# Performance work log

Hardware: AMD Instinct MI355X
Metric: run time of the kernel (lower is better)

Reference implementation:

```python
import jax, jax.numpy as jnp
import numpy as np


def setup_inputs() -> dict:
    key = jax.random.key(0)
    ks = jax.random.split(key, 5)
    N, D, H, E = 8192, 1024, 4096, 8
    s = 0.02
    return {
        "x": jax.random.normal(ks[0], (N, D), jnp.float32),
        "Wr": jax.random.normal(ks[1], (D, E), jnp.float32) * s,
        "br": jnp.zeros((E,), jnp.float32),
        "W1": jax.random.normal(ks[2], (E, D, H), jnp.float32) * s,
        "b1": jnp.zeros((E, H), jnp.float32),
        "W2": jax.random.normal(ks[3], (E, H, D), jnp.float32) * s,
        "b2": jnp.zeros((E, D), jnp.float32),
        "k": 2,
    }


def reference(x, Wr, br, W1, b1, W2, b2, k):
    # Router (eval mode: no gate noise)
    logits = x @ Wr + br                      # [N, E]
    scores = jax.nn.softmax(logits, axis=-1)  # [N, E]
    topk_vals, topk_inds = jax.lax.top_k(scores, k)  # [N, k]
    N, E = scores.shape
    # dispatch_mask: zeros scattered with top-k probabilities
    dispatch_mask = jnp.zeros_like(scores).at[
        jnp.arange(N)[:, None], topk_inds
    ].set(topk_vals)                          # [N, E]
    # Dense all-expert FFN compute (faithful to the original wasteful pattern)
    h = jax.nn.relu(jnp.einsum('nd,edh->neh', x, W1) + b1)   # [N, E, H]
    expert_outputs = jnp.einsum('neh,ehd->ned', h, W2) + b2  # [N, E, D]
    output = jnp.einsum('ned,ne->nd', expert_outputs, dispatch_mask)  # [N, D]
    # Load-balancing aux loss (torch.var is unbiased, ddof=1)
    importance = dispatch_mask.sum(axis=0)    # [E]
    imp_mean = jnp.mean(importance)
    imp_var = jnp.var(importance, ddof=1)
    aux_loss = imp_var / (imp_mean ** 2 + 1e-9)
    return output, aux_loss
```

## Files before the change

kernel.cpp:

```cpp
#include <hip/hip_runtime.h>
#include <hip/hip_bf16.h>


#define NTOK 8192
#define DDIM 1024
#define HDIM 4096
#define NEXP 8
#define NASSIGN (NTOK * 2)
#define MAX_MT 72
#define GRID1 (16 * MAX_MT)
#define GRID2A (4 * 2 * MAX_MT)
#define GRID2B (4 * MAX_MT)

typedef __bf16 bf16_t;
typedef __bf16 bf16x2 __attribute__((ext_vector_type(2)));
typedef __bf16 bf16x4 __attribute__((ext_vector_type(4)));
typedef __bf16 bf16x8 __attribute__((ext_vector_type(8)));
typedef float f32x4 __attribute__((ext_vector_type(4)));

#define GLOAD16(gptr, lptr)                                                    \
  __builtin_amdgcn_global_load_lds(                                            \
      (const __attribute__((address_space(1))) void*)(gptr),                   \
      (__attribute__((address_space(3))) void*)(lptr), 16, 0, 0)

#define VMCNT0 asm volatile("s_waitcnt vmcnt(0)" ::: "memory")

#define MFMA16(a, b, c) __builtin_amdgcn_mfma_f32_16x16x32_bf16(a, b, c, 0, 0, 0)

__device__ __forceinline__ int xcd_swz(int orig, int nwg) {
  const int cpx = nwg >> 3;
  return (orig & 7) * cpx + (orig >> 3);
}

__global__ void __launch_bounds__(256) transpose_cvt_kernel(
    const float* __restrict__ in, bf16_t* __restrict__ out, int R, int C) {
  __shared__ float tile[64][33];
  const size_t mat = (size_t)R * C;
  const float* ip = in + (size_t)blockIdx.z * mat;
  bf16_t* op = out + (size_t)blockIdx.z * mat;
  const int c0 = blockIdx.x * 32, r0 = blockIdx.y * 64;
  const int tx = threadIdx.x, ty = threadIdx.y;
#pragma unroll
  for (int i = 0; i < 8; ++i) {
    const int r = ty + 8 * i;
    tile[r][tx] = ip[(size_t)(r0 + r) * C + (c0 + tx)];
  }
  __syncthreads();
#pragma unroll
  for (int j = 0; j < 4; ++j) {
    const int c = ty + 8 * j;
    bf16x2 v;
    v[0] = (bf16_t)tile[2 * tx][c];
    v[1] = (bf16_t)tile[2 * tx + 1][c];
    *(bf16x2*)(op + (size_t)(c0 + c) * R + r0 + 2 * tx) = v;
  }
}

__global__ void __launch_bounds__(256) router_kernel(
    const float* __restrict__ x, const float* __restrict__ Wr,
    const float* __restrict__ br, int2* __restrict__ ids,
    float2* __restrict__ prs, int* __restrict__ counts,
    bf16_t* __restrict__ xb) {
  const int n = blockIdx.x;
  const int t = threadIdx.x;
  const int wave = t >> 6, lane = t & 63;
  const float4 xv = ((const float4*)(x + (size_t)n * DDIM))[t];
  bf16x4 o;
  o[0] = (bf16_t)xv.x; o[1] = (bf16_t)xv.y;
  o[2] = (bf16_t)xv.z; o[3] = (bf16_t)xv.w;
  ((bf16x4*)(xb + (size_t)n * DDIM))[t] = o;

  float acc[NEXP];
#pragma unroll
  for (int e = 0; e < NEXP; ++e) acc[e] = 0.f;
  const float xq[4] = {xv.x, xv.y, xv.z, xv.w};
#pragma unroll
  for (int q = 0; q < 4; ++q) {
    const float* w = Wr + (size_t)(4 * t + q) * NEXP;
#pragma unroll
    for (int e = 0; e < NEXP; ++e) acc[e] += xq[q] * w[e];
  }
#pragma unroll
  for (int off = 32; off >= 1; off >>= 1)
#pragma unroll
    for (int e = 0; e < NEXP; ++e) acc[e] += __shfl_down(acc[e], off);
  __shared__ float red[4][NEXP];
  if (lane == 0)
#pragma unroll
    for (int e = 0; e < NEXP; ++e) red[wave][e] = acc[e];
  __syncthreads();
  if (t == 0) {
    float l[NEXP];
#pragma unroll
    for (int e = 0; e < NEXP; ++e)
      l[e] = ((red[0][e] + red[1][e]) + (red[2][e] + red[3][e])) + br[e];
    int i1 = 0; float v1 = l[0];
    for (int e = 1; e < NEXP; ++e)
      if (l[e] > v1) { v1 = l[e]; i1 = e; }
    int i2 = (i1 == 0) ? 1 : 0; float v2 = l[i2];
    for (int e = 0; e < NEXP; ++e)
      if (e != i1 && l[e] > v2) { v2 = l[e]; i2 = e; }
    float denom = 0.f;
    for (int e = 0; e < NEXP; ++e) denom += expf(l[e] - v1);
    ids[n] = make_int2(i1, i2);
    prs[n] = make_float2(1.f / denom, expf(v2 - v1) / denom);
    atomicAdd(&counts[i1], 1);
    atomicAdd(&counts[i2], 1);
  }
}

__global__ void __launch_bounds__(256) scan_aux_kernel(
    const int* __restrict__ counts, int* __restrict__ offsets,
    int* __restrict__ tmap, const int2* __restrict__ ids,
    const float2* __restrict__ prs, float* __restrict__ aux_out) {
  const int t = threadIdx.x;
  if (t == 0) {
    int off = 0, nt = 0;
    for (int e = 0; e < NEXP; ++e) {
      offsets[e] = off;
      const int c = counts[e];
      for (int m0 = 0; m0 < c; m0 += 256) {
        tmap[nt] = e;
        tmap[MAX_MT + nt] = m0;
        ++nt;
      }
      off += c;
    }
    offsets[NEXP] = off;
    tmap[2 * MAX_MT] = nt;
  }
  float imp[NEXP];
#pragma unroll
  for (int e = 0; e < NEXP; ++e) imp[e] = 0.f;
  for (int n = t; n < NTOK; n += 256) {
    const int2 id = ids[n];
    const float2 pr = prs[n];
#pragma unroll
    for (int e = 0; e < NEXP; ++e)
      imp[e] += (id.x == e ? pr.x : 0.f) + (id.y == e ? pr.y : 0.f);
  }
  __shared__ float red[256][NEXP];
#pragma unroll
  for (int e = 0; e < NEXP; ++e) red[t][e] = imp[e];
  __syncthreads();
  for (int s = 128; s >= 1; s >>= 1) {
    if (t < s) {
#pragma unroll
      for (int e = 0; e < NEXP; ++e) red[t][e] += red[t + s][e];
    }
    __syncthreads();
  }
  if (t == 0) {
    float m = 0.f;
    for (int e = 0; e < NEXP; ++e) m += red[0][e];
    m *= (1.f / NEXP);
    float v = 0.f;
    for (int e = 0; e < NEXP; ++e) {
      const float d = red[0][e] - m;
      v += d * d;
    }
    v *= (1.f / (NEXP - 1));
    aux_out[0] = v / (m * m + 1e-9f);
  }
}

__global__ void __launch_bounds__(256) scatter_kernel(
    const int2* __restrict__ ids, const float2* __restrict__ prs,
    const int* __restrict__ offsets, int* __restrict__ cursor,
    int* __restrict__ btok, float* __restrict__ bprob,
    int2* __restrict__ amap) {
  const int n = blockIdx.x * 256 + threadIdx.x;
  if (n >= NTOK) return;
  const int2 id = ids[n];
  const float2 pr = prs[n];
  int p = atomicAdd(&cursor[id.x], 1);
  const int a1 = offsets[id.x] + p;
  btok[a1] = n;
  bprob[a1] = pr.x;
  p = atomicAdd(&cursor[id.y], 1);
  const int a2 = offsets[id.y] + p;
  btok[a2] = n;
  bprob[a2] = pr.y;
  amap[n] = make_int2(a1, a2);
}

__global__ void __launch_bounds__(256) combine_kernel(
    const float* __restrict__ o0, const float* __restrict__ o1,
    const int2* __restrict__ amap, const float* __restrict__ bprob,
    float* __restrict__ out) {
  const int n = blockIdx.x;
  const int d = threadIdx.x * 4;
  const int2 a = amap[n];
  const float p1 = bprob[a.x], p2 = bprob[a.y];
  const float4 u0 = *(const float4*)(o0 + (size_t)a.x * DDIM + d);
  const float4 u1 = *(const float4*)(o1 + (size_t)a.x * DDIM + d);
  const float4 v0 = *(const float4*)(o0 + (size_t)a.y * DDIM + d);
  const float4 v1 = *(const float4*)(o1 + (size_t)a.y * DDIM + d);
  float4 r;
  r.x = p1 * (u0.x + u1.x) + p2 * (v0.x + v1.x);
  r.y = p1 * (u0.y + u1.y) + p2 * (v0.y + v1.y);
  r.z = p1 * (u0.z + u1.z) + p2 * (v0.z + v1.z);
  r.w = p1 * (u0.w + u1.w) + p2 * (v0.w + v1.w);
  *(float4*)(out + (size_t)n * DDIM + d) = r;
}


#define STAGE_A(BUF, KO)                                                       \
  GLOAD16(asrc0 + (KO), (char*)Al + (BUF)*32768 + 0*8192 + wave*1024);         \
  GLOAD16(asrc1 + (KO), (char*)Al + (BUF)*32768 + 1*8192 + wave*1024);         \
  GLOAD16(asrc2 + (KO), (char*)Al + (BUF)*32768 + 2*8192 + wave*1024);         \
  GLOAD16(asrc3 + (KO), (char*)Al + (BUF)*32768 + 3*8192 + wave*1024);

#define STAGE_B(BUF, KO)                                                       \
  GLOAD16(bsrc0 + (KO), (char*)Bl + (BUF)*32768 + 0*8192 + wave*1024);         \
  GLOAD16(bsrc1 + (KO), (char*)Bl + (BUF)*32768 + 1*8192 + wave*1024);         \
  GLOAD16(bsrc2 + (KO), (char*)Bl + (BUF)*32768 + 2*8192 + wave*1024);         \
  GLOAD16(bsrc3 + (KO), (char*)Bl + (BUF)*32768 + 3*8192 + wave*1024);

#define LOAD_AF(O0, O1, O2, O3, KX)                                            \
  af0 = *(const bf16x8*)(Ac + ((O0) ^ (KX)));                                  \
  af1 = *(const bf16x8*)(Ac + ((O1) ^ (KX)));                                  \
  af2 = *(const bf16x8*)(Ac + ((O2) ^ (KX)));                                  \
  af3 = *(const bf16x8*)(Ac + ((O3) ^ (KX)));

#define LOAD_BF(KX)                                                            \
  bf0 = *(const bf16x8*)(Bc + (boffb0 ^ (KX)));                                \
  bf1 = *(const bf16x8*)(Bc + (boffb1 ^ (KX)));                                \
  bf2 = *(const bf16x8*)(Bc + (boffb2 ^ (KX)));                                \
  bf3 = *(const bf16x8*)(Bc + (boffb3 ^ (KX)));

#define MROW(M, A)                                                             \
  acc[M][0] = MFMA16(A, bf0, acc[M][0]);                                       \
  acc[M][1] = MFMA16(A, bf1, acc[M][1]);                                       \
  acc[M][2] = MFMA16(A, bf2, acc[M][2]);                                       \
  acc[M][3] = MFMA16(A, bf3, acc[M][3]);

#define PH_MFMA(MB)                                                            \
  __builtin_amdgcn_s_setprio(1);                                               \
  MROW(MB + 0, af0) MROW(MB + 1, af1) MROW(MB + 2, af2) MROW(MB + 3, af3)      \
  __builtin_amdgcn_s_setprio(0);

#define PH_ENTER                                                               \
  __builtin_amdgcn_sched_barrier(0x1);                                         \
  __builtin_amdgcn_s_barrier();

#define PH_EXIT __builtin_amdgcn_s_barrier();

#define KLOOP(NT)                                                              \
  STAGE_A(0, 0)                                                                \
  STAGE_B(0, 0)                                                                \
  VMCNT0;                                                                      \
  __builtin_amdgcn_s_barrier();                                                \
  __builtin_amdgcn_sched_barrier(0);                                           \
  _Pragma("unroll 2") for (int t = 0; t < (NT); ++t) {                         \
    const int cb = t & 1, nc = cb ^ 1;                                         \
    const int ko = (t + 1) * 64;                                               \
    const char* Ac = (const char*)Al + cb * 32768;                             \
    const char* Bc = (const char*)Bl + cb * 32768;                             \
    const bool pf = (t + 1 < (NT));                                            \
    bf16x8 af0, af1, af2, af3, bf0, bf1, bf2, bf3;                             \
                               \
    LOAD_AF(aoffb0, aoffb1, aoffb2, aoffb3, 0)                                 \
    LOAD_BF(0)                                                                 \
    if (pf) { STAGE_A(nc, ko) }                                                \
    PH_ENTER                                                                   \
    PH_MFMA(0)                                                                 \
    PH_EXIT                                                                    \
                                        \
    LOAD_AF(aoffb4, aoffb5, aoffb6, aoffb7, 0)                                 \
    if (pf) { STAGE_B(nc, ko) }                                                \
    PH_ENTER                                                                   \
    PH_MFMA(4)                                                                 \
    PH_EXIT                                                                    \
                                             \
    LOAD_AF(aoffb0, aoffb1, aoffb2, aoffb3, 64)                                \
    LOAD_BF(64)                                                                \
    PH_ENTER                                                                   \
    PH_MFMA(0)                                                                 \
    PH_EXIT                                                                    \
                                 \
    LOAD_AF(aoffb4, aoffb5, aoffb6, aoffb7, 64)                                \
    PH_ENTER                                                                   \
    PH_MFMA(4)                                                                 \
    VMCNT0;                                                                    \
    __builtin_amdgcn_s_barrier();                                              \
    __builtin_amdgcn_sched_barrier(0);                                         \
  }

#define GEOM_SETUP                                                             \
  const int tid = threadIdx.x;                                                 \
  const int wave = tid >> 6;                                                   \
  const int lane = tid & 63;                                                   \
  const int wr = (wave >> 2) * 128;                                            \
  const int wc = (wave & 3) * 64;                                              \
  const int lrow = lane & 15;                                                  \
  const int lslot = lane >> 4;                                                 \
  const int sxor = ((lslot ^ (lrow & 7)) << 4);                                \
  const int aoffb0 = (wr + 0 * 16 + lrow) * 128 + sxor;                        \
  const int aoffb1 = (wr + 1 * 16 + lrow) * 128 + sxor;                        \
  const int aoffb2 = (wr + 2 * 16 + lrow) * 128 + sxor;                        \
  const int aoffb3 = (wr + 3 * 16 + lrow) * 128 + sxor;                        \
  const int aoffb4 = (wr + 4 * 16 + lrow) * 128 + sxor;                        \
  const int aoffb5 = (wr + 5 * 16 + lrow) * 128 + sxor;                        \
  const int aoffb6 = (wr + 6 * 16 + lrow) * 128 + sxor;                        \
  const int aoffb7 = (wr + 7 * 16 + lrow) * 128 + sxor;                        \
  const int boffb0 = (wc + 0 * 16 + lrow) * 128 + sxor;                        \
  const int boffb1 = (wc + 1 * 16 + lrow) * 128 + sxor;                        \
  const int boffb2 = (wc + 2 * 16 + lrow) * 128 + sxor;                        \
  const int boffb3 = (wc + 3 * 16 + lrow) * 128 + sxor;

#define SRC_ROW(S) ((S)*64 + (tid >> 3))
#define SRC_SLOT ((tid & 7))

__global__ void __launch_bounds__(512, 2) gemm1_kernel(
    const bf16_t* __restrict__ xb, const bf16_t* __restrict__ W1t,
    const float* __restrict__ b1, const int* __restrict__ btok,
    const int* __restrict__ offsets, const int* __restrict__ counts,
    const int* __restrict__ tmap, bf16_t* __restrict__ h) {
  const int job = xcd_swz((int)blockIdx.x, GRID1);
  const int tidx = job >> 4;
  const int nblk = job & 15;
  if (tidx >= tmap[2 * MAX_MT]) return;
  const int e = tmap[tidx];
  const int m0 = tmap[MAX_MT + tidx];
  const int cnt = counts[e];
  const int aoff = offsets[e];
  const int n0 = nblk * 256;

  __shared__ __align__(16) bf16_t Al[2][256 * 64];
  __shared__ __align__(16) bf16_t Bl[2][256 * 64];

  GEOM_SETUP

  const bf16_t *asrc0, *asrc1, *asrc2, *asrc3;
  const bf16_t *bsrc0, *bsrc1, *bsrc2, *bsrc3;
  {
    const int p = SRC_SLOT;
#pragma unroll
    for (int s = 0; s < 4; ++s) {
      const int row = SRC_ROW(s);
      const int l = p ^ (row & 7);
      int arow = m0 + row;
      if (arow > cnt - 1) arow = cnt - 1;
      const bf16_t* ap = xb + (size_t)btok[aoff + arow] * DDIM + l * 8;
      const bf16_t* bp = W1t + ((size_t)e * HDIM + n0 + row) * DDIM + l * 8;
      if (s == 0) { asrc0 = ap; bsrc0 = bp; }
      else if (s == 1) { asrc1 = ap; bsrc1 = bp; }
      else if (s == 2) { asrc2 = ap; bsrc2 = bp; }
      else { asrc3 = ap; bsrc3 = bp; }
    }
  }

  f32x4 acc[8][4];
#pragma unroll
  for (int mf = 0; mf < 8; ++mf)
#pragma unroll
    for (int nf = 0; nf < 4; ++nf) acc[mf][nf] = (f32x4){0.f, 0.f, 0.f, 0.f};

  KLOOP(16)

  const int rbase = (lane >> 4) * 4;
  const float* b1e = b1 + (size_t)e * HDIM + n0;
#pragma unroll
  for (int nf = 0; nf < 4; ++nf) {
    const int cl = wc + nf * 16 + lrow;
    const float bb = b1e[cl];
#pragma unroll
    for (int mf = 0; mf < 8; ++mf) {
#pragma unroll
      for (int r = 0; r < 4; ++r) {
        const int grow = wr + mf * 16 + rbase + r;
        if (m0 + grow < cnt)
          h[(size_t)(aoff + m0 + grow) * HDIM + (n0 + cl)] =
              (bf16_t)fmaxf(acc[mf][nf][r] + bb, 0.f);
      }
    }
  }
}

template <int NT, int KSP, bool ATOMIC>
__global__ void __launch_bounds__(512, 2) gemm2_kernel(
    const bf16_t* __restrict__ h, const bf16_t* __restrict__ W2t,
    const float* __restrict__ b2, const int* __restrict__ btok,
    const float* __restrict__ bprob, const int* __restrict__ offsets,
    const int* __restrict__ counts, const int* __restrict__ tmap,
    float* __restrict__ o0, float* __restrict__ o1,
    float* __restrict__ out) {
  const int nwg = 4 * KSP * MAX_MT;
  const int job = xcd_swz((int)blockIdx.x, nwg);
  const int tidx = job / (4 * KSP);
  const int rem = job % (4 * KSP);
  const int nblk = rem & 3;
  const int kch = rem >> 2;
  if (tidx >= tmap[2 * MAX_MT]) return;
  const int e = tmap[tidx];
  const int m0 = tmap[MAX_MT + tidx];
  const int cnt = counts[e];
  const int aoff = offsets[e];
  const int n0 = nblk * 256;
  const int kbase = kch * (HDIM / KSP);

  __shared__ __align__(16) bf16_t Al[2][256 * 64];
  __shared__ __align__(16) bf16_t Bl[2][256 * 64];

  GEOM_SETUP

  const bf16_t *asrc0, *asrc1, *asrc2, *asrc3;
  const bf16_t *bsrc0, *bsrc1, *bsrc2, *bsrc3;
  {
    const int p = SRC_SLOT;
#pragma unroll
    for (int s = 0; s < 4; ++s) {
      const int row = SRC_ROW(s);
      const int l = p ^ (row & 7);
      int arow = m0 + row;
      if (arow > cnt - 1) arow = cnt - 1;
      const bf16_t* ap = h + (size_t)(aoff + arow) * HDIM + kbase + l * 8;
      const bf16_t* bp =
          W2t + ((size_t)e * DDIM + n0 + row) * HDIM + kbase + l * 8;
      if (s == 0) { asrc0 = ap; bsrc0 = bp; }
      else if (s == 1) { asrc1 = ap; bsrc1 = bp; }
      else if (s == 2) { asrc2 = ap; bsrc2 = bp; }
      else { asrc3 = ap; bsrc3 = bp; }
    }
  }

  f32x4 acc[8][4];
#pragma unroll
  for (int mf = 0; mf < 8; ++mf)
#pragma unroll
    for (int nf = 0; nf < 4; ++nf) acc[mf][nf] = (f32x4){0.f, 0.f, 0.f, 0.f};

  KLOOP(NT)

  const int rbase = (lane >> 4) * 4;
  const float* b2e = b2 + (size_t)e * DDIM + n0;
  float bb[4];
#pragma unroll
  for (int nf = 0; nf < 4; ++nf)
    bb[nf] = (kch == 0) ? b2e[wc + nf * 16 + lrow] : 0.f;

  if (ATOMIC) {
#pragma unroll
    for (int mf = 0; mf < 8; ++mf) {
#pragma unroll
      for (int r = 0; r < 4; ++r) {
        const int grow = wr + mf * 16 + rbase + r;
        if (m0 + grow < cnt) {
          const int assign = aoff + m0 + grow;
          const int tok = btok[assign];
          const float p = bprob[assign];
          float* orow = out + (size_t)tok * DDIM + n0;
#pragma unroll
          for (int nf = 0; nf < 4; ++nf) {
            const int cl = wc + nf * 16 + lrow;
            atomicAdd(&orow[cl], (acc[mf][nf][r] + bb[nf]) * p);
          }
        }
      }
    }
  } else {
    float* obase = (kch == 0) ? o0 : o1;
#pragma unroll
    for (int mf = 0; mf < 8; ++mf) {
#pragma unroll
      for (int r = 0; r < 4; ++r) {
        const int grow = wr + mf * 16 + rbase + r;
        if (m0 + grow < cnt) {
          const int assign = aoff + m0 + grow;
          float* orow = obase + (size_t)assign * DDIM + n0;
#pragma unroll
          for (int nf = 0; nf < 4; ++nf) {
            const int cl = wc + nf * 16 + lrow;
            orow[cl] = acc[mf][nf][r] + bb[nf];
          }
        }
      }
    }
  }
}


extern "C" void kernel_launch(void* const* d_in, const int* in_sizes, int n_in,
                              void* d_out, int out_size, void* d_ws,
                              size_t ws_size, hipStream_t stream) {
  const float* x = (const float*)d_in[0];
  const float* Wr = (const float*)d_in[1];
  const float* br = (const float*)d_in[2];
  const float* W1 = (const float*)d_in[3];
  const float* b1 = (const float*)d_in[4];
  const float* W2 = (const float*)d_in[5];
  const float* b2 = (const float*)d_in[6];

  char* w = (char*)d_ws;
  auto alloc = [&](size_t bytes) -> char* {
    char* p = w;
    w += (bytes + 255) & ~(size_t)255;
    return p;
  };
  bf16_t* xb = (bf16_t*)alloc((size_t)NTOK * DDIM * 2);
  bf16_t* W1t = (bf16_t*)alloc((size_t)NEXP * DDIM * HDIM * 2);
  bf16_t* W2t = (bf16_t*)alloc((size_t)NEXP * DDIM * HDIM * 2);
  bf16_t* hbuf = (bf16_t*)alloc((size_t)NASSIGN * HDIM * 2);
  int* btok = (int*)alloc(NASSIGN * 4);
  float* bprob = (float*)alloc(NASSIGN * 4);
  int2* ids = (int2*)alloc(NTOK * 8);
  float2* prs = (float2*)alloc(NTOK * 8);
  int2* amap = (int2*)alloc(NTOK * 8);
  int* ctrl = (int*)alloc(64);
  int* offsets = (int*)alloc(64);
  int* tmap = (int*)alloc((2 * MAX_MT + 1) * 4);
  int* counts = ctrl;
  int* cursor = ctrl + 8;
  const size_t osz = (size_t)NASSIGN * DDIM * 4;
  float* o0 = (float*)alloc(osz);
  float* o1 = (float*)d_ws;
  const size_t needed = (size_t)(w - (char*)d_ws);
  const bool pathA = ws_size >= needed;
  (void)in_sizes; (void)n_in;

  float* out = (float*)d_out;

  hipMemsetAsync(ctrl, 0, 64, stream);
  if (!pathA)
    hipMemsetAsync(d_out, 0, (size_t)out_size * 4, stream);

  transpose_cvt_kernel<<<dim3(HDIM / 32, DDIM / 64, NEXP), dim3(32, 8), 0,
                         stream>>>(W1, W1t, DDIM, HDIM);
  transpose_cvt_kernel<<<dim3(DDIM / 32, HDIM / 64, NEXP), dim3(32, 8), 0,
                         stream>>>(W2, W2t, HDIM, DDIM);
  router_kernel<<<NTOK, 256, 0, stream>>>(x, Wr, br, ids, prs, counts, xb);
  scan_aux_kernel<<<1, 256, 0, stream>>>(counts, offsets, tmap, ids, prs,
                                         out + (size_t)NTOK * DDIM);
  scatter_kernel<<<NTOK / 256, 256, 0, stream>>>(ids, prs, offsets, cursor,
                                                 btok, bprob, amap);
  gemm1_kernel<<<GRID1, 512, 0, stream>>>(xb, W1t, b1, btok, offsets, counts,
                                          tmap, hbuf);
  if (pathA) {
    gemm2_kernel<32, 2, false><<<GRID2A, 512, 0, stream>>>(
        hbuf, W2t, b2, btok, bprob, offsets, counts, tmap, o0, o1, out);
    combine_kernel<<<NTOK, 256, 0, stream>>>(o0, o1, amap, bprob, out);
  } else {
    gemm2_kernel<64, 1, true><<<GRID2B, 512, 0, stream>>>(
        hbuf, W2t, b2, btok, bprob, offsets, counts, tmap, o0, o1, out);
  }
}
```

Before: 824.8 us.

## Restructure GEMM k-loop into quarter-tile staged pipeline with partial vmcnt waits

Replaces the double-buffered k-loop in both expert GEMMs with a finer-grained schedule. Global-to-LDS loads are issued in 64-row quarter tiles spread across the four MFMA phases, and the loop waits with partial vmcnt counts instead of draining all loads. The LDS layout is reorganised into 64-row blocks indexed per wave half and quarter, and the last iteration is peeled so the loop has no prefetch predicate. The aim is to overlap memory loads with MFMA work and cut full-drain stalls, at the cost of more complex ordering that depends on the vmcnt counts being correct.

```diff
diff --git a/kernel.cpp b/kernel.cpp
--- a/kernel.cpp
+++ b/kernel.cpp
@@ -23,7 +23,10 @@
       (const __attribute__((address_space(1))) void*)(gptr),                   \
       (__attribute__((address_space(3))) void*)(lptr), 16, 0, 0)
 
-#define VMCNT0 asm volatile("s_waitcnt vmcnt(0)" ::: "memory")
+#define VMCNT(n) asm volatile("s_waitcnt vmcnt(" #n ")" ::: "memory")
+#define BAR                                                                    \
+  __builtin_amdgcn_s_barrier();                                                \
+  __builtin_amdgcn_sched_barrier(0);
 
 #define MFMA16(a, b, c) __builtin_amdgcn_mfma_f32_16x16x32_bf16(a, b, c, 0, 0, 0)
 
@@ -205,112 +208,126 @@
 }
 
 
-#define STAGE_A(BUF, KO)                                                       \
-  GLOAD16(asrc0 + (KO), (char*)Al + (BUF)*32768 + 0*8192 + wave*1024);         \
-  GLOAD16(asrc1 + (KO), (char*)Al + (BUF)*32768 + 1*8192 + wave*1024);         \
-  GLOAD16(asrc2 + (KO), (char*)Al + (BUF)*32768 + 2*8192 + wave*1024);         \
-  GLOAD16(asrc3 + (KO), (char*)Al + (BUF)*32768 + 3*8192 + wave*1024);
-
-#define STAGE_B(BUF, KO)                                                       \
-  GLOAD16(bsrc0 + (KO), (char*)Bl + (BUF)*32768 + 0*8192 + wave*1024);         \
-  GLOAD16(bsrc1 + (KO), (char*)Bl + (BUF)*32768 + 1*8192 + wave*1024);         \
-  GLOAD16(bsrc2 + (KO), (char*)Bl + (BUF)*32768 + 2*8192 + wave*1024);         \
-  GLOAD16(bsrc3 + (KO), (char*)Bl + (BUF)*32768 + 3*8192 + wave*1024);
-
-#define LOAD_AF(O0, O1, O2, O3, KX)                                            \
-  af0 = *(const bf16x8*)(Ac + ((O0) ^ (KX)));                                  \
-  af1 = *(const bf16x8*)(Ac + ((O1) ^ (KX)));                                  \
-  af2 = *(const bf16x8*)(Ac + ((O2) ^ (KX)));                                  \
-  af3 = *(const bf16x8*)(Ac + ((O3) ^ (KX)));
-
-#define LOAD_BF(KX)                                                            \
-  bf0 = *(const bf16x8*)(Bc + (boffb0 ^ (KX)));                                \
-  bf1 = *(const bf16x8*)(Bc + (boffb1 ^ (KX)));                                \
-  bf2 = *(const bf16x8*)(Bc + (boffb2 ^ (KX)));                                \
-  bf3 = *(const bf16x8*)(Bc + (boffb3 ^ (KX)));
-
-#define MROW(M, A)                                                             \
-  acc[M][0] = MFMA16(A, bf0, acc[M][0]);                                       \
-  acc[M][1] = MFMA16(A, bf1, acc[M][1]);                                       \
-  acc[M][2] = MFMA16(A, bf2, acc[M][2]);                                       \
-  acc[M][3] = MFMA16(A, bf3, acc[M][3]);
-
-#define PH_MFMA(MB)                                                            \
+#define ISSUE_A_Q0(NB, KO)                                                     \
+  GLOAD16(aS00 + (KO), (char*)Al + ((NB)*4 + 0) * 8192 + wave * 1024);         \
+  GLOAD16(aS10 + (KO), (char*)Al + ((NB)*4 + 2) * 8192 + wave * 1024);
+#define ISSUE_A_Q1(NB, KO)                                                     \
+  GLOAD16(aS01 + (KO), (char*)Al + ((NB)*4 + 1) * 8192 + wave * 1024);         \
+  GLOAD16(aS11 + (KO), (char*)Al + ((NB)*4 + 3) * 8192 + wave * 1024);
+#define ISSUE_B_01(NB, KO)                                                     \
+  GLOAD16(bS0 + (KO), (char*)Bl + ((NB)*4 + 0) * 8192 + wave * 1024);          \
+  GLOAD16(bS1 + (KO), (char*)Bl + ((NB)*4 + 1) * 8192 + wave * 1024);
+#define ISSUE_B_23(NB, KO)                                                     \
+  GLOAD16(bS2 + (KO), (char*)Bl + ((NB)*4 + 2) * 8192 + wave * 1024);          \
+  GLOAD16(bS3 + (KO), (char*)Bl + ((NB)*4 + 3) * 8192 + wave * 1024);
+
+#define READ_FA(QOFF, KX)                                                      \
+  fa0 = *(const bf16x8*)(Ac + (QOFF) + (off0 ^ (KX)));                         \
+  fa1 = *(const bf16x8*)(Ac + (QOFF) + (off1 ^ (KX)));                         \
+  fa2 = *(const bf16x8*)(Ac + (QOFF) + (off2 ^ (KX)));                         \
+  fa3 = *(const bf16x8*)(Ac + (QOFF) + (off3 ^ (KX)));
+#define READ_G0                                                                \
+  g00 = *(const bf16x8*)(Bc + off0);                                           \
+  g01 = *(const bf16x8*)(Bc + off1);                                           \
+  g02 = *(const bf16x8*)(Bc + off2);                                           \
+  g03 = *(const bf16x8*)(Bc + off3);
+#define READ_G1                                                                \
+  g10 = *(const bf16x8*)(Bc + (off0 ^ 64));                                    \
+  g11 = *(const bf16x8*)(Bc + (off1 ^ 64));                                    \
+  g12 = *(const bf16x8*)(Bc + (off2 ^ 64));                                    \
+  g13 = *(const bf16x8*)(Bc + (off3 ^ 64));
+
+#define MROW(M, A, G0, G1, G2, G3)                                             \
+  acc[M][0] = MFMA16(A, G0, acc[M][0]);                                        \
+  acc[M][1] = MFMA16(A, G1, acc[M][1]);                                        \
+  acc[M][2] = MFMA16(A, G2, acc[M][2]);                                        \
+  acc[M][3] = MFMA16(A, G3, acc[M][3]);
+#define MFMA_BLK0(MB)                                                          \
   __builtin_amdgcn_s_setprio(1);                                               \
-  MROW(MB + 0, af0) MROW(MB + 1, af1) MROW(MB + 2, af2) MROW(MB + 3, af3)      \
+  MROW(MB + 0, fa0, g00, g01, g02, g03)                                        \
+  MROW(MB + 1, fa1, g00, g01, g02, g03)                                        \
+  MROW(MB + 2, fa2, g00, g01, g02, g03)                                        \
+  MROW(MB + 3, fa3, g00, g01, g02, g03)                                        \
   __builtin_amdgcn_s_setprio(0);
-
-#define PH_ENTER                                                               \
-  __builtin_amdgcn_sched_barrier(0x1);                                         \
-  __builtin_amdgcn_s_barrier();
-
-#define PH_EXIT __builtin_amdgcn_s_barrier();
+#define MFMA_BLK1(MB)                                                          \
+  __builtin_amdgcn_s_setprio(1);                                               \
+  MROW(MB + 0, fa0, g10, g11, g12, g13)                                        \
+  MROW(MB + 1, fa1, g10, g11, g12, g13)                                        \
+  MROW(MB + 2, fa2, g10, g11, g12, g13)                                        \
+  MROW(MB + 3, fa3, g10, g11, g12, g13)                                        \
+  __builtin_amdgcn_s_setprio(0);
 
 #define KLOOP(NT)                                                              \
-  STAGE_A(0, 0)                                                                \
-  STAGE_B(0, 0)                                                                \
-  VMCNT0;                                                                      \
-  __builtin_amdgcn_s_barrier();                                                \
-  __builtin_amdgcn_sched_barrier(0);                                           \
-  _Pragma("unroll 2") for (int t = 0; t < (NT); ++t) {                         \
-    const int cb = t & 1, nc = cb ^ 1;                                         \
+  ISSUE_A_Q0(0, 0) ISSUE_B_01(0, 0) ISSUE_B_23(0, 0) ISSUE_A_Q1(0, 0)          \
+  VMCNT(2);                                                                    \
+  BAR                                                                          \
+  _Pragma("unroll 1") for (int t = 0; t < (NT)-1; ++t) {                       \
+    const int cb = t & 1, nb = cb ^ 1;                                         \
     const int ko = (t + 1) * 64;                                               \
-    const char* Ac = (const char*)Al + cb * 32768;                             \
-    const char* Bc = (const char*)Bl + cb * 32768;                             \
-    const bool pf = (t + 1 < (NT));                                            \
-    bf16x8 af0, af1, af2, af3, bf0, bf1, bf2, bf3;                             \
-                               \
-    LOAD_AF(aoffb0, aoffb1, aoffb2, aoffb3, 0)                                 \
-    LOAD_BF(0)                                                                 \
-    if (pf) { STAGE_A(nc, ko) }                                                \
-    PH_ENTER                                                                   \
-    PH_MFMA(0)                                                                 \
-    PH_EXIT                                                                    \
-                                        \
-    LOAD_AF(aoffb4, aoffb5, aoffb6, aoffb7, 0)                                 \
-    if (pf) { STAGE_B(nc, ko) }                                                \
-    PH_ENTER                                                                   \
-    PH_MFMA(4)                                                                 \
-    PH_EXIT                                                                    \
-                                             \
-    LOAD_AF(aoffb0, aoffb1, aoffb2, aoffb3, 64)                                \
-    LOAD_BF(64)                                                                \
-    PH_ENTER                                                                   \
-    PH_MFMA(0)                                                                 \
-    PH_EXIT                                                                    \
-                                 \
-    LOAD_AF(aoffb4, aoffb5, aoffb6, aoffb7, 64)                                \
-    PH_ENTER                                                                   \
-    PH_MFMA(4)                                                                 \
-    VMCNT0;                                                                    \
-    __builtin_amdgcn_s_barrier();                                              \
-    __builtin_amdgcn_sched_barrier(0);                                         \
+    const char* Ac = (const char*)Al + cb * 32768 + mh * 16384;                \
+    const char* Bc = (const char*)Bl + cb * 32768 + nq * 8192;                 \
+    bf16x8 fa0, fa1, fa2, fa3;                                                 \
+    bf16x8 g00, g01, g02, g03, g10, g11, g12, g13;                             \
+    READ_FA(0, 0)                                                              \
+    READ_G0                                                                    \
+    ISSUE_A_Q0(nb, ko)                                                         \
+    MFMA_BLK0(0)                                                               \
+    BAR                                                                        \
+    READ_FA(0, 64)                                                             \
+    READ_G1                                                                    \
+    ISSUE_B_01(nb, ko)                                                         \
+    MFMA_BLK1(0)                                                               \
+    VMCNT(4);                                                                  \
+    BAR                                                                        \
+    READ_FA(8192, 0)                                                           \
+    ISSUE_B_23(nb, ko)                                                         \
+    MFMA_BLK0(4)                                                               \
+    BAR                                                                        \
+    READ_FA(8192, 64)                                                          \
+    ISSUE_A_Q1(nb, ko)                                                         \
+    MFMA_BLK1(4)                                                               \
+    VMCNT(2);                                                                  \
+    BAR                                                                        \
+  }                                                                            \
+  {                                                                            \
+    const int cb = ((NT)-1) & 1;                                               \
+    const char* Ac = (const char*)Al + cb * 32768 + mh * 16384;                \
+    const char* Bc = (const char*)Bl + cb * 32768 + nq * 8192;                 \
+    bf16x8 fa0, fa1, fa2, fa3;                                                 \
+    bf16x8 g00, g01, g02, g03, g10, g11, g12, g13;                             \
+    READ_FA(0, 0)                                                              \
+    READ_G0                                                                    \
+    MFMA_BLK0(0)                                                               \
+    BAR                                                                        \
+    READ_FA(0, 64)                                                             \
+    READ_G1                                                                    \
+    MFMA_BLK1(0)                                                               \
+    VMCNT(0);                                                                  \
+    BAR                                                                        \
+    READ_FA(8192, 0)                                                           \
+    MFMA_BLK0(4)                                                               \
+    BAR                                                                        \
+    READ_FA(8192, 64)                                                          \
+    MFMA_BLK1(4)                                                               \
   }
 
 #define GEOM_SETUP                                                             \
   const int tid = threadIdx.x;                                                 \
   const int wave = tid >> 6;                                                   \
   const int lane = tid & 63;                                                   \
-  const int wr = (wave >> 2) * 128;                                            \
-  const int wc = (wave & 3) * 64;                                              \
+  const int mh = wave >> 2;                                                    \
+  const int nq = wave & 3;                                                     \
+  const int wr = mh * 128;                                                     \
+  const int wc = nq * 64;                                                      \
   const int lrow = lane & 15;                                                  \
   const int lslot = lane >> 4;                                                 \
   const int sxor = ((lslot ^ (lrow & 7)) << 4);                                \
-  const int aoffb0 = (wr + 0 * 16 + lrow) * 128 + sxor;                        \
-  const int aoffb1 = (wr + 1 * 16 + lrow) * 128 + sxor;                        \
-  const int aoffb2 = (wr + 2 * 16 + lrow) * 128 + sxor;                        \
-  const int aoffb3 = (wr + 3 * 16 + lrow) * 128 + sxor;                        \
-  const int aoffb4 = (wr + 4 * 16 + lrow) * 128 + sxor;                        \
-  const int aoffb5 = (wr + 5 * 16 + lrow) * 128 + sxor;                        \
-  const int aoffb6 = (wr + 6 * 16 + lrow) * 128 + sxor;                        \
-  const int aoffb7 = (wr + 7 * 16 + lrow) * 128 + sxor;                        \
-  const int boffb0 = (wc + 0 * 16 + lrow) * 128 + sxor;                        \
-  const int boffb1 = (wc + 1 * 16 + lrow) * 128 + sxor;                        \
-  const int boffb2 = (wc + 2 * 16 + lrow) * 128 + sxor;                        \
-  const int boffb3 = (wc + 3 * 16 + lrow) * 128 + sxor;
-
-#define SRC_ROW(S) ((S)*64 + (tid >> 3))
-#define SRC_SLOT ((tid & 7))
+  const int off0 = (0 * 16 + lrow) * 128 + sxor;                               \
+  const int off1 = (1 * 16 + lrow) * 128 + sxor;                               \
+  const int off2 = (2 * 16 + lrow) * 128 + sxor;                               \
+  const int off3 = (3 * 16 + lrow) * 128 + sxor;                               \
+  const int srow = tid >> 3;                                                   \
+  const int slsl = ((tid & 7) ^ (srow & 7)) * 8;
 
 __global__ void __launch_bounds__(512, 2) gemm1_kernel(
     const bf16_t* __restrict__ xb, const bf16_t* __restrict__ W1t,
@@ -327,29 +344,24 @@
   const int aoff = offsets[e];
   const int n0 = nblk * 256;
 
-  __shared__ __align__(16) bf16_t Al[2][256 * 64];
-  __shared__ __align__(16) bf16_t Bl[2][256 * 64];
+  __shared__ __align__(16) bf16_t Al[8 * 64 * 64];
+  __shared__ __align__(16) bf16_t Bl[8 * 64 * 64];
 
   GEOM_SETUP
 
-  const bf16_t *asrc0, *asrc1, *asrc2, *asrc3;
-  const bf16_t *bsrc0, *bsrc1, *bsrc2, *bsrc3;
-  {
-    const int p = SRC_SLOT;
-#pragma unroll
-    for (int s = 0; s < 4; ++s) {
-      const int row = SRC_ROW(s);
-      const int l = p ^ (row & 7);
-      int arow = m0 + row;
-      if (arow > cnt - 1) arow = cnt - 1;
-      const bf16_t* ap = xb + (size_t)btok[aoff + arow] * DDIM + l * 8;
-      const bf16_t* bp = W1t + ((size_t)e * HDIM + n0 + row) * DDIM + l * 8;
-      if (s == 0) { asrc0 = ap; bsrc0 = bp; }
-      else if (s == 1) { asrc1 = ap; bsrc1 = bp; }
-      else if (s == 2) { asrc2 = ap; bsrc2 = bp; }
-      else { asrc3 = ap; bsrc3 = bp; }
-    }
-  }
+  auto aSrc = [&](int rit) {
+    int arow = m0 + rit;
+    if (arow > cnt - 1) arow = cnt - 1;
+    return xb + (size_t)btok[aoff + arow] * DDIM + slsl;
+  };
+  const bf16_t* aS00 = aSrc(0 + srow);
+  const bf16_t* aS01 = aSrc(64 + srow);
+  const bf16_t* aS10 = aSrc(128 + srow);
+  const bf16_t* aS11 = aSrc(192 + srow);
+  const bf16_t* bS0 = W1t + ((size_t)e * HDIM + n0 + 0 + srow) * DDIM + slsl;
+  const bf16_t* bS1 = W1t + ((size_t)e * HDIM + n0 + 64 + srow) * DDIM + slsl;
+  const bf16_t* bS2 = W1t + ((size_t)e * HDIM + n0 + 128 + srow) * DDIM + slsl;
+  const bf16_t* bS3 = W1t + ((size_t)e * HDIM + n0 + 192 + srow) * DDIM + slsl;
 
   f32x4 acc[8][4];
 #pragma unroll
@@ -400,30 +412,28 @@
   const int n0 = nblk * 256;
   const int kbase = kch * (HDIM / KSP);
 
-  __shared__ __align__(16) bf16_t Al[2][256 * 64];
-  __shared__ __align__(16) bf16_t Bl[2][256 * 64];
+  __shared__ __align__(16) bf16_t Al[8 * 64 * 64];
+  __shared__ __align__(16) bf16_t Bl[8 * 64 * 64];
 
   GEOM_SETUP
 
-  const bf16_t *asrc0, *asrc1, *asrc2, *asrc3;
-  const bf16_t *bsrc0, *bsrc1, *bsrc2, *bsrc3;
-  {
-    const int p = SRC_SLOT;
-#pragma unroll
-    for (int s = 0; s < 4; ++s) {
-      const int row = SRC_ROW(s);
-      const int l = p ^ (row & 7);
-      int arow = m0 + row;
-      if (arow > cnt - 1) arow = cnt - 1;
-      const bf16_t* ap = h + (size_t)(aoff + arow) * HDIM + kbase + l * 8;
-      const bf16_t* bp =
-          W2t + ((size_t)e * DDIM + n0 + row) * HDIM + kbase + l * 8;
-      if (s == 0) { asrc0 = ap; bsrc0 = bp; }
-      else if (s == 1) { asrc1 = ap; bsrc1 = bp; }
-      else if (s == 2) { asrc2 = ap; bsrc2 = bp; }
-      else { asrc3 = ap; bsrc3 = bp; }
-    }
-  }
+  auto aSrc = [&](int rit) {
+    int arow = m0 + rit;
+    if (arow > cnt - 1) arow = cnt - 1;
+    return h + (size_t)(aoff + arow) * HDIM + kbase + slsl;
+  };
+  const bf16_t* aS00 = aSrc(0 + srow);
+  const bf16_t* aS01 = aSrc(64 + srow);
+  const bf16_t* aS10 = aSrc(128 + srow);
+  const bf16_t* aS11 = aSrc(192 + srow);
+  const bf16_t* bS0 =
+      W2t + ((size_t)e * DDIM + n0 + 0 + srow) * HDIM + kbase + slsl;
+  const bf16_t* bS1 =
+      W2t + ((size_t)e * DDIM + n0 + 64 + srow) * HDIM + kbase + slsl;
+  const bf16_t* bS2 =
+      W2t + ((size_t)e * DDIM + n0 + 128 + srow) * HDIM + kbase + slsl;
+  const bf16_t* bS3 =
+      W2t + ((size_t)e * DDIM + n0 + 192 + srow) * HDIM + kbase + slsl;
 
   f32x4 acc[8][4];
 #pragma unroll
```

After: 840.3 us (median of 4 runs). Within noise of the previous version (+1.9%).
